# Kernel tuning notes

Hardware: AMD Instinct MI355X
Metric: run time of the kernel (lower is better)

Reference implementation:

```python
import jax, jax.numpy as jnp
import numpy as np

D_MODEL = 64     # input_dim // 4
D_INNER = 128    # expand * d_model
D_STATE = 16
D_CONV = 4
DT_RANK = 4      # ceil(d_model / 16)
EPS = 1e-5


def layernorm(x, g, b):
    m = x.mean(-1, keepdims=True)
    v = x.var(-1, keepdims=True)
    return (x - m) * jax.lax.rsqrt(v + EPS) * g + b


def mamba(u, W_in, W_conv, b_conv, W_xproj, W_dt, b_dt, A_log, Dp, W_out):
    # u: [B, L, d_model]
    B, L, _ = u.shape
    xz = u @ W_in.T                              # [B, L, 2*d_inner]
    xi, z = xz[..., :D_INNER], xz[..., D_INNER:]
    # depthwise causal conv1d over L
    xp = jnp.pad(xi, ((0, 0), (D_CONV - 1, 0), (0, 0)))
    xc = b_conv + sum(xp[:, k:k + L, :] * W_conv[:, k] for k in range(D_CONV))
    xc = jax.nn.silu(xc)                         # [B, L, d_inner]
    proj = xc @ W_xproj.T                        # [B, L, dt_rank + 2*d_state]
    dtp = proj[..., :DT_RANK]
    Bm = proj[..., DT_RANK:DT_RANK + D_STATE]    # [B, L, d_state]
    Cm = proj[..., DT_RANK + D_STATE:]           # [B, L, d_state]
    dt = jax.nn.softplus(dtp @ W_dt.T + b_dt)    # [B, L, d_inner]
    A = -jnp.exp(A_log)                          # [d_inner, d_state]
    dA = jnp.exp(dt[..., None] * A)              # [B, L, d_inner, d_state]
    dBx = (dt * xc)[..., None] * Bm[:, :, None, :]

    def step(h, t):
        dA_t, dBx_t, C_t = t
        h = dA_t * h + dBx_t                     # [B, d_inner, d_state]
        return h, jnp.einsum('bds,bs->bd', h, C_t)

    h0 = jnp.zeros((B, D_INNER, D_STATE), u.dtype)
    _, ys = jax.lax.scan(step, h0, (dA.transpose(1, 0, 2, 3),
                                    dBx.transpose(1, 0, 2, 3),
                                    Cm.transpose(1, 0, 2)))
    y = ys.transpose(1, 0, 2) + Dp * xc          # [B, L, d_inner]
    y = y * jax.nn.silu(z)
    return y @ W_out.T                           # [B, L, d_model]


def _forward(x, x1, x2, x3, g1, be1, g2, be2, g3, be3, g4, be4, skip_scale,
             W_in, W_conv, b_conv, W_xproj, W_dt, b_dt, A_log, D, W_out):
    Bb, C = x.shape[:2]
    img_dims = x2.shape[2:]
    mparams = (W_in, W_conv, b_conv, W_xproj, W_dt, b_dt, A_log, D, W_out)

    def branch(inp, g, b):
        xf = inp.reshape(Bb, C, -1).transpose(0, 2, 1)   # [B, L, C]
        xn = layernorm(xf, g, b)
        return mamba(xn, *mparams) + skip_scale * xn

    x_mamba = jnp.concatenate([branch(x, g1, be1), branch(x1, g2, be2),
                               branch(x2, g3, be3), branch(x3, g4, be4)], axis=2)
    out = x_mamba.transpose(0, 2, 1).reshape(Bb, 4 * C, *img_dims)
    return out


def setup_inputs():
    key = jax.random.key(0)
    ks = jax.random.split(key, 12)
    f = lambda k, shp, s=1.0: jax.random.normal(k, shp, dtype=jnp.float32) * s
    inp = {
        'x': f(ks[0], (8, 64, 32, 32)),
        'x1': f(ks[1], (8, 64, 32, 32)),
        'x2': f(ks[2], (8, 64, 32, 32)),
        'x3': f(ks[3], (8, 64, 32, 32)),
        'g1': jnp.ones(64), 'be1': jnp.zeros(64),
        'g2': jnp.ones(64), 'be2': jnp.zeros(64),
        'g3': jnp.ones(64), 'be3': jnp.zeros(64),
        'g4': jnp.ones(64), 'be4': jnp.zeros(64),
        'skip_scale': jnp.ones((1,), jnp.float32),
        'W_in': f(ks[4], (2 * D_INNER, D_MODEL), 0.1),
        'W_conv': f(ks[5], (D_INNER, D_CONV), 0.3),
        'b_conv': jnp.zeros(D_INNER),
        'W_xproj': f(ks[6], (DT_RANK + 2 * D_STATE, D_INNER), 0.1),
        'W_dt': f(ks[7], (D_INNER, DT_RANK), 0.1),
        'b_dt': f(ks[8], (D_INNER,), 0.1),
        'A_log': jnp.log(jnp.tile(jnp.arange(1, D_STATE + 1, dtype=jnp.float32), (D_INNER, 1))),
        'D': jnp.ones(D_INNER),
        'W_out': f(ks[9], (D_MODEL, D_INNER), 0.1),
    }
    return inp


def reference(x, x1, x2, x3, g1, be1, g2, be2, g3, be3, g4, be4, skip_scale,
              W_in, W_conv, b_conv, W_xproj, W_dt, b_dt, A_log, D, W_out):
    return _forward(x, x1, x2, x3, g1, be1, g2, be2, g3, be3, g4, be4, skip_scale,
                    W_in, W_conv, b_conv, W_xproj, W_dt, b_dt, A_log, D, W_out)
```

## Files before the change

### kernel.cpp

```cpp
#include <hip/hip_runtime.h>
#include <hip/hip_bf16.h>

#define L2E 1.4426950408889634f
#define LN2 0.6931471805599453f

__device__ __forceinline__ float fexp2(float x) { return __builtin_amdgcn_exp2f(x); }
__device__ __forceinline__ float flog2(float x) { return __builtin_amdgcn_logf(x); }
__device__ __forceinline__ int uniform(int x) { return __builtin_amdgcn_readfirstlane(x); }
__device__ __forceinline__ float sigmoidf_(float v) { return 1.f / (1.f + fexp2(-v * L2E)); }
__device__ __forceinline__ float softplusf_(float t) {
    return (t > 20.f) ? t : LN2 * flog2(1.f + fexp2(t * L2E));
}

constexpr size_t O_M   = 0;
constexpr size_t O_RS  = 32768;
constexpr size_t O_G   = 65536;
constexpr size_t O_Z   = 4259840;
constexpr size_t O_XC  = 8454144;
constexpr size_t O_BM  = 12648448;
constexpr size_t O_CM  = 13172736;
constexpr size_t O_DTP = 13697024;
constexpr size_t O_HP  = 13828096;

__global__ __launch_bounds__(256) void k1_ln_inproj(
    const float* __restrict__ x0, const float* __restrict__ x1,
    const float* __restrict__ x2, const float* __restrict__ x3,
    const float* __restrict__ win,
    const float* __restrict__ g1, const float* __restrict__ be1,
    const float* __restrict__ g2, const float* __restrict__ be2,
    const float* __restrict__ g3, const float* __restrict__ be3,
    const float* __restrict__ g4, const float* __restrict__ be4,
    float* __restrict__ ws)
{
    __shared__ float sX[64 * 68];
    __shared__ float sW[64 * 68];
    __shared__ float sM[64], sR[64];
    int bid = blockIdx.x;
    int seq = bid >> 6, jb = (bid >> 4) & 3, pb = bid & 15;
    int branch = seq >> 3, b = seq & 7;
    int tid = threadIdx.x;
    int lane = tid & 63;
    int wq = uniform(tid >> 6);
    const float* xin = (branch==0)?x0:(branch==1)?x1:(branch==2)?x2:x3;
    const float* gam = (branch==0)?g1:(branch==1)?g2:(branch==2)?g3:g4;
    const float* bet = (branch==0)?be1:(branch==1)?be2:(branch==2)?be3:be4;
    const float* xb = xin + (size_t)b * 65536;

#pragma unroll
    for (int r = 0; r < 16; ++r) {
        int row = r * 4 + wq;
        sX[row * 68 + lane] = xb[(size_t)row * 1024 + pb * 64 + lane];
        sW[lane * 68 + row] = win[(size_t)(jb * 64 + row) * 64 + lane];
    }
    __syncthreads();
    if (tid < 64) {
        float sum = 0.f, sq = 0.f;
#pragma unroll
        for (int c = 0; c < 64; ++c) {
            float v = sX[c * 68 + tid];
            sum += v; sq += v * v;
        }
        float mean = sum * (1.f/64.f);
        float var  = sq * (1.f/64.f) - mean * mean;
        float rs   = rsqrtf(var + 1e-5f);
        sM[tid] = mean; sR[tid] = rs;
        if (jb == 0) {
            ws[O_M  + (size_t)seq * 1024 + pb * 64 + tid] = mean;
            ws[O_RS + (size_t)seq * 1024 + pb * 64 + tid] = rs;
        }
    }
    __syncthreads();
#pragma unroll
    for (int r = 0; r < 16; ++r) {
        int c = r * 4 + wq;
        float v = sX[c * 68 + lane];
        sX[c * 68 + lane] = (v - sM[lane]) * sR[lane] * gam[c] + bet[c];
    }
    __syncthreads();
    int jt = tid >> 4, pt = tid & 15;
    float acc[4][4];
#pragma unroll
    for (int i = 0; i < 4; ++i)
#pragma unroll
        for (int j = 0; j < 4; ++j) acc[i][j] = 0.f;
    for (int c = 0; c < 64; ++c) {
        float4 wv = *(const float4*)&sW[c * 68 + jt * 4];
        float4 xv = *(const float4*)&sX[c * 68 + pt * 4];
        float w[4] = {wv.x, wv.y, wv.z, wv.w};
        float x[4] = {xv.x, xv.y, xv.z, xv.w};
#pragma unroll
        for (int i = 0; i < 4; ++i)
#pragma unroll
            for (int j = 0; j < 4; ++j) acc[i][j] += w[i] * x[j];
    }
    int p0 = pb * 64 + pt * 4;
    float* xi = ws + O_G + (size_t)seq * 131072;
    float* zz = ws + O_Z + (size_t)seq * 131072;
#pragma unroll
    for (int ji = 0; ji < 4; ++ji) {
        int j = jb * 64 + jt * 4 + ji;
        float4 v = make_float4(acc[ji][0], acc[ji][1], acc[ji][2], acc[ji][3]);
        if (j < 128) *(float4*)&xi[(size_t)j * 1024 + p0] = v;
        else         *(float4*)&zz[(size_t)(j - 128) * 1024 + p0] = v;
    }
}

__global__ __launch_bounds__(256) void k2_conv_proj(
    const float* __restrict__ wconv, const float* __restrict__ bconv,
    const float* __restrict__ wxp, float* __restrict__ ws)
{
    __shared__ float sWx[128 * 40];
    __shared__ float sAcc[36 * 64];
    int bid = blockIdx.x;
    int seq = bid >> 4, ptile = bid & 15;
    int tid = threadIdx.x;
    int lane = tid & 63;
    int wq = uniform(tid >> 6);
    int p = ptile * 64 + lane;

    for (int i = tid; i < 36 * 64; i += 256) sAcc[i] = 0.f;
    for (int i = tid; i < 36 * 128; i += 256) {
        int j = i >> 7, d = i & 127;
        sWx[d * 40 + j] = wxp[i];
    }
    __syncthreads();

    const float* xirow = ws + O_G  + (size_t)seq * 131072;
    float*       xcrow = ws + O_XC + (size_t)seq * 131072;
    float acc36[36];
#pragma unroll
    for (int j = 0; j < 36; ++j) acc36[j] = 0.f;

    for (int dd = 0; dd < 32; ++dd) {
        int d = wq * 32 + dd;
        const float* row = xirow + (size_t)d * 1024;
        float4 wc = *(const float4*)&wconv[d * 4];
        float v = bconv[d];
        v += ((p >= 3) ? row[p-3] : 0.f) * wc.x;
        v += ((p >= 2) ? row[p-2] : 0.f) * wc.y;
        v += ((p >= 1) ? row[p-1] : 0.f) * wc.z;
        v += row[p] * wc.w;
        v = v * sigmoidf_(v);
        xcrow[(size_t)d * 1024 + p] = v;
#pragma unroll
        for (int jq = 0; jq < 9; ++jq) {
            float4 w4 = *(const float4*)&sWx[d * 40 + jq * 4];
            acc36[jq*4+0] += v * w4.x;
            acc36[jq*4+1] += v * w4.y;
            acc36[jq*4+2] += v * w4.z;
            acc36[jq*4+3] += v * w4.w;
        }
    }
#pragma unroll
    for (int j = 0; j < 36; ++j) atomicAdd(&sAcc[j * 64 + lane], acc36[j]);
    __syncthreads();
    if (tid < 64) {
        int pp = ptile * 64 + tid;
        float* Bm = ws + O_BM + (size_t)seq * 16384;
        float* Cm = ws + O_CM + (size_t)seq * 16384;
        for (int j = 0; j < 36; ++j) {
            float t = sAcc[j * 64 + tid];
            if (j < 4)       ws[O_DTP + ((size_t)seq * 1024 + pp) * 4 + j] = t;
            else if (j < 20) Bm[(size_t)(j - 4)  * 1024 + pp] = t;
            else             Cm[(size_t)(j - 20) * 1024 + pp] = t;
        }
    }
}

__device__ __forceinline__ void k3_preload(const float* wdt, const float* bdt,
                                           const float* alog, int d0, int s0,
                                           float4& wdt0, float4& wdt1, float& bdt0, float& bdt1,
                                           float* a2)
{
    wdt0 = *(const float4*)(wdt + d0 * 4);
    wdt1 = *(const float4*)(wdt + (d0 + 1) * 4);
    bdt0 = bdt[d0]; bdt1 = bdt[d0 + 1];
    float4 a0 = *(const float4*)(alog + d0 * 16 + s0);
    float4 a1 = *(const float4*)(alog + (d0 + 1) * 16 + s0);
    a2[0] = -fexp2(a0.x * L2E) * L2E; a2[1] = -fexp2(a0.y * L2E) * L2E;
    a2[2] = -fexp2(a0.z * L2E) * L2E; a2[3] = -fexp2(a0.w * L2E) * L2E;
    a2[4] = -fexp2(a1.x * L2E) * L2E; a2[5] = -fexp2(a1.y * L2E) * L2E;
    a2[6] = -fexp2(a1.z * L2E) * L2E; a2[7] = -fexp2(a1.w * L2E) * L2E;
}

__global__ __launch_bounds__(256) void k3a_scan(const float* __restrict__ wdt,
                                                const float* __restrict__ bdt,
                                                const float* __restrict__ alog,
                                                float* __restrict__ ws)
{
    __shared__ float sXC[128 * 33];
    __shared__ __align__(16) float sB[32 * 16];
    __shared__ __align__(16) float sDtp[32 * 4];
    int bid = blockIdx.x;
    int seq = bid >> 5, ch = bid & 31;
    int lb = ch * 32;
    int tid = threadIdx.x;
    int d0 = (tid >> 2) * 2, s0 = (tid & 3) * 4;

    float4 wdt0, wdt1; float bdt0, bdt1; float a2[8];
    k3_preload(wdt, bdt, alog, d0, s0, wdt0, wdt1, bdt0, bdt1, a2);

    const float* xcg = ws + O_XC + (size_t)seq * 131072;
    const float* Bmg = ws + O_BM + (size_t)seq * 16384;
    for (int i = tid; i < 4096; i += 256) {
        int d = i >> 5, li = i & 31;
        sXC[d * 33 + li] = xcg[(size_t)d * 1024 + lb + li];
    }
    for (int i = tid; i < 512; i += 256) {
        int s = i >> 5, li = i & 31;
        sB[li * 16 + s] = Bmg[(size_t)s * 1024 + lb + li];
    }
    if (tid < 128) sDtp[tid] = ws[O_DTP + ((size_t)seq * 1024 + lb + (tid >> 2)) * 4 + (tid & 3)];
    __syncthreads();

    float h[8];
#pragma unroll
    for (int i = 0; i < 8; ++i) h[i] = 0.f;
    float sdt0 = 0.f, sdt1 = 0.f;
    for (int li = 0; li < 32; ++li) {
        float4 q = *(const float4*)&sDtp[li * 4];
        float dt0 = softplusf_(bdt0 + q.x*wdt0.x + q.y*wdt0.y + q.z*wdt0.z + q.w*wdt0.w);
        float dt1 = softplusf_(bdt1 + q.x*wdt1.x + q.y*wdt1.y + q.z*wdt1.z + q.w*wdt1.w);
        float xc0 = sXC[d0 * 33 + li], xc1 = sXC[(d0 + 1) * 33 + li];
        float dx0 = dt0 * xc0, dx1 = dt1 * xc1;
        float4 Bv = *(const float4*)&sB[li * 16 + s0];
        float bv[4] = {Bv.x, Bv.y, Bv.z, Bv.w};
        sdt0 += dt0; sdt1 += dt1;
#pragma unroll
        for (int ss = 0; ss < 4; ++ss) {
            float e0 = fexp2(dt0 * a2[ss]);
            h[ss] = e0 * h[ss] + dx0 * bv[ss];
            float e1 = fexp2(dt1 * a2[4 + ss]);
            h[4 + ss] = e1 * h[4 + ss] + dx1 * bv[ss];
        }
    }
    float* hp = ws + O_HP + (size_t)(seq * 32 + ch) * 4096;
#pragma unroll
    for (int ss = 0; ss < 4; ++ss) {
        hp[d0 * 16 + s0 + ss]            = fexp2(a2[ss] * sdt0);
        hp[(d0 + 1) * 16 + s0 + ss]      = fexp2(a2[4 + ss] * sdt1);
        hp[2048 + d0 * 16 + s0 + ss]     = h[ss];
        hp[2048 + (d0 + 1) * 16 + s0 + ss] = h[4 + ss];
    }
}

__global__ __launch_bounds__(256) void k3b_compose(float* __restrict__ ws)
{
    int seq = blockIdx.x;
    int tid = threadIdx.x;
    int d0 = (tid >> 2) * 2, s0 = (tid & 3) * 4;
    int i0 = d0 * 16 + s0, i1 = (d0 + 1) * 16 + s0;
    float h[8];
#pragma unroll
    for (int i = 0; i < 8; ++i) h[i] = 0.f;
    float* hpb = ws + O_HP + (size_t)seq * 32 * 4096;
    for (int c = 0; c < 32; ++c) {
        float* hp = hpb + (size_t)c * 4096;
        float4 P0 = *(const float4*)&hp[i0];
        float4 P1 = *(const float4*)&hp[i1];
        float4 E0 = *(const float4*)&hp[2048 + i0];
        float4 E1 = *(const float4*)&hp[2048 + i1];
        *(float4*)&hp[i0] = make_float4(h[0], h[1], h[2], h[3]);
        *(float4*)&hp[i1] = make_float4(h[4], h[5], h[6], h[7]);
        h[0] = P0.x * h[0] + E0.x; h[1] = P0.y * h[1] + E0.y;
        h[2] = P0.z * h[2] + E0.z; h[3] = P0.w * h[3] + E0.w;
        h[4] = P1.x * h[4] + E1.x; h[5] = P1.y * h[5] + E1.y;
        h[6] = P1.z * h[6] + E1.z; h[7] = P1.w * h[7] + E1.w;
    }
}

__global__ __launch_bounds__(256) void k3c_scan_y(const float* __restrict__ wdt,
                                                  const float* __restrict__ bdt,
                                                  const float* __restrict__ alog,
                                                  float* __restrict__ ws)
{
    __shared__ float sXC[128 * 33];
    __shared__ float sY[128 * 33];
    __shared__ __align__(16) float sB[32 * 16];
    __shared__ __align__(16) float sC[32 * 16];
    __shared__ __align__(16) float sDtp[32 * 4];
    int bid = blockIdx.x;
    int seq = bid >> 5, ch = bid & 31;
    int lb = ch * 32;
    int tid = threadIdx.x;
    int sq = tid & 3;
    int d0 = (tid >> 2) * 2, s0 = sq * 4;

    float4 wdt0, wdt1; float bdt0, bdt1; float a2[8];
    k3_preload(wdt, bdt, alog, d0, s0, wdt0, wdt1, bdt0, bdt1, a2);

    const float* xcg = ws + O_XC + (size_t)seq * 131072;
    const float* Bmg = ws + O_BM + (size_t)seq * 16384;
    const float* Cmg = ws + O_CM + (size_t)seq * 16384;
    float*       gg  = ws + O_G  + (size_t)seq * 131072;
    for (int i = tid; i < 4096; i += 256) {
        int d = i >> 5, li = i & 31;
        sXC[d * 33 + li] = xcg[(size_t)d * 1024 + lb + li];
    }
    for (int i = tid; i < 512; i += 256) {
        int s = i >> 5, li = i & 31;
        sB[li * 16 + s] = Bmg[(size_t)s * 1024 + lb + li];
        sC[li * 16 + s] = Cmg[(size_t)s * 1024 + lb + li];
    }
    if (tid < 128) sDtp[tid] = ws[O_DTP + ((size_t)seq * 1024 + lb + (tid >> 2)) * 4 + (tid & 3)];

    const float* hp = ws + O_HP + (size_t)(seq * 32 + ch) * 4096;
    float4 H0 = *(const float4*)&hp[d0 * 16 + s0];
    float4 H1 = *(const float4*)&hp[(d0 + 1) * 16 + s0];
    float h[8] = {H0.x, H0.y, H0.z, H0.w, H1.x, H1.y, H1.z, H1.w};
    __syncthreads();

    for (int li = 0; li < 32; ++li) {
        float4 q = *(const float4*)&sDtp[li * 4];
        float dt0 = softplusf_(bdt0 + q.x*wdt0.x + q.y*wdt0.y + q.z*wdt0.z + q.w*wdt0.w);
        float dt1 = softplusf_(bdt1 + q.x*wdt1.x + q.y*wdt1.y + q.z*wdt1.z + q.w*wdt1.w);
        float xc0 = sXC[d0 * 33 + li], xc1 = sXC[(d0 + 1) * 33 + li];
        float dx0 = dt0 * xc0, dx1 = dt1 * xc1;
        float4 Bv = *(const float4*)&sB[li * 16 + s0];
        float4 Cv = *(const float4*)&sC[li * 16 + s0];
        float bv[4] = {Bv.x, Bv.y, Bv.z, Bv.w};
        float cv[4] = {Cv.x, Cv.y, Cv.z, Cv.w};
        float acc0 = 0.f, acc1 = 0.f;
#pragma unroll
        for (int ss = 0; ss < 4; ++ss) {
            float e0 = fexp2(dt0 * a2[ss]);
            h[ss] = e0 * h[ss] + dx0 * bv[ss];
            acc0 += h[ss] * cv[ss];
            float e1 = fexp2(dt1 * a2[4 + ss]);
            h[4 + ss] = e1 * h[4 + ss] + dx1 * bv[ss];
            acc1 += h[4 + ss] * cv[ss];
        }
        acc0 += __shfl_xor(acc0, 1); acc0 += __shfl_xor(acc0, 2);
        acc1 += __shfl_xor(acc1, 1); acc1 += __shfl_xor(acc1, 2);
        if (sq == 0) {
            sY[d0 * 33 + li]       = acc0;
            sY[(d0 + 1) * 33 + li] = acc1;
        }
    }
    __syncthreads();
    for (int i = tid; i < 4096; i += 256) {
        int d = i >> 5, li = i & 31;
        gg[(size_t)d * 1024 + lb + li] = sY[d * 33 + li];
    }
}

__global__ __launch_bounds__(256) void k4_out(
    const float* __restrict__ x0, const float* __restrict__ x1,
    const float* __restrict__ x2, const float* __restrict__ x3,
    const float* __restrict__ g1, const float* __restrict__ be1,
    const float* __restrict__ g2, const float* __restrict__ be2,
    const float* __restrict__ g3, const float* __restrict__ be3,
    const float* __restrict__ g4, const float* __restrict__ be4,
    const float* __restrict__ dpar, const float* __restrict__ woutp,
    const float* __restrict__ skipp, const float* __restrict__ ws,
    float* __restrict__ out)
{
    __shared__ float sG[64 * 68];
    __shared__ float sW[64 * 68];
    int bid = blockIdx.x;
    int seq = bid >> 4, pb = bid & 15;
    int branch = seq >> 3, b = seq & 7;
    int tid = threadIdx.x;
    int lane = tid & 63;
    int wq = uniform(tid >> 6);
    int ct = tid >> 4, pt = tid & 15;

    const float* ys = ws + O_G  + (size_t)seq * 131072;
    const float* zz = ws + O_Z  + (size_t)seq * 131072;
    const float* xc = ws + O_XC + (size_t)seq * 131072;

    float acc[4][4];
#pragma unroll
    for (int i = 0; i < 4; ++i)
#pragma unroll
        for (int j = 0; j < 4; ++j) acc[i][j] = 0.f;

    for (int hf = 0; hf < 2; ++hf) {
#pragma unroll
        for (int r = 0; r < 16; ++r) {
            int row = r * 4 + wq;
            sW[lane * 68 + row] = woutp[(size_t)row * 128 + hf * 64 + lane];
            int d = hf * 64 + row;
            size_t off = (size_t)d * 1024 + pb * 64 + lane;
            float yv = ys[off], zv = zz[off], xcv = xc[off];
            sG[row * 68 + lane] = (yv + dpar[d] * xcv) * (zv * sigmoidf_(zv));
        }
        __syncthreads();
        for (int dl = 0; dl < 64; ++dl) {
            float4 wv = *(const float4*)&sW[dl * 68 + ct * 4];
            float4 gv = *(const float4*)&sG[dl * 68 + pt * 4];
            float w[4] = {wv.x, wv.y, wv.z, wv.w};
            float g[4] = {gv.x, gv.y, gv.z, gv.w};
#pragma unroll
            for (int i = 0; i < 4; ++i)
#pragma unroll
                for (int j = 0; j < 4; ++j) acc[i][j] += w[i] * g[j];
        }
        __syncthreads();
    }

    const float* xin = (branch==0)?x0:(branch==1)?x1:(branch==2)?x2:x3;
    const float* gam = (branch==0)?g1:(branch==1)?g2:(branch==2)?g3:g4;
    const float* bet = (branch==0)?be1:(branch==1)?be2:(branch==2)?be3:be4;
    const float* xb = xin + (size_t)b * 65536;
    int p0 = pb * 64 + pt * 4;
    float skipv = skipp[0];
    float4 m4 = *(const float4*)&ws[O_M  + (size_t)seq * 1024 + p0];
    float4 r4 = *(const float4*)&ws[O_RS + (size_t)seq * 1024 + p0];
    float mm[4] = {m4.x, m4.y, m4.z, m4.w};
    float rr[4] = {r4.x, r4.y, r4.z, r4.w};
#pragma unroll
    for (int ci = 0; ci < 4; ++ci) {
        int c = ct * 4 + ci;
        float4 xv = *(const float4*)&xb[(size_t)c * 1024 + p0];
        float xvv[4] = {xv.x, xv.y, xv.z, xv.w};
        float gc = gam[c], bc = bet[c];
        float o[4];
#pragma unroll
        for (int pi = 0; pi < 4; ++pi) {
            float xn = (xvv[pi] - mm[pi]) * rr[pi] * gc + bc;
            o[pi] = acc[ci][pi] + skipv * xn;
        }
        *(float4*)&out[((size_t)b * 256 + branch * 64 + c) * 1024 + p0] =
            make_float4(o[0], o[1], o[2], o[3]);
    }
}

extern "C" void kernel_launch(void* const* d_in, const int* in_sizes, int n_in,
                              void* d_out, int out_size, void* d_ws, size_t ws_size,
                              hipStream_t stream) {
    float* ws = (float*)d_ws;
    auto f = [&](int i) { return (const float*)d_in[i]; };
    hipLaunchKernelGGL(k1_ln_inproj, dim3(2048), dim3(256), 0, stream,
        f(0), f(1), f(2), f(3), f(13),
        f(4), f(5), f(6), f(7), f(8), f(9), f(10), f(11), ws);
    hipLaunchKernelGGL(k2_conv_proj, dim3(512), dim3(256), 0, stream,
        f(14), f(15), f(16), ws);
    hipLaunchKernelGGL(k3a_scan, dim3(1024), dim3(256), 0, stream, f(17), f(18), f(19), ws);
    hipLaunchKernelGGL(k3b_compose, dim3(32), dim3(256), 0, stream, ws);
    hipLaunchKernelGGL(k3c_scan_y, dim3(1024), dim3(256), 0, stream, f(17), f(18), f(19), ws);
    hipLaunchKernelGGL(k4_out, dim3(512), dim3(256), 0, stream,
        f(0), f(1), f(2), f(3),
        f(4), f(5), f(6), f(7), f(8), f(9), f(10), f(11),
        f(20), f(21), f(12), ws, (float*)d_out);
}
```

Measured before the change: 245.1 us.

## Stage conv inputs in LDS and split x_proj outputs across waves

The conv+x_proj kernel now loads each input row tile (with a three-element halo) into shared memory once, computes the causal conv from LDS, and writes the SiLU result back into the same LDS buffer. The x_proj matvec is then restructured so each wave owns 9 of the 36 output channels over all 128 channels, reading weights as uniform scalar loads. This replaces the earlier per-wave partial sums and 36 LDS atomics per thread plus the serialized 64-thread store loop. It adds an extra barrier and a 128x68 LDS buffer, and relies on the weight loads being scalarized.

```diff
diff --git a/kernel.cpp b/kernel.cpp
--- a/kernel.cpp
+++ b/kernel.cpp
@@ -109,61 +109,66 @@
     const float* __restrict__ wconv, const float* __restrict__ bconv,
     const float* __restrict__ wxp, float* __restrict__ ws)
 {
-    __shared__ float sWx[128 * 40];
-    __shared__ float sAcc[36 * 64];
+    __shared__ float sX[128 * 68];
     int bid = blockIdx.x;
     int seq = bid >> 4, ptile = bid & 15;
     int tid = threadIdx.x;
     int lane = tid & 63;
     int wq = uniform(tid >> 6);
-    int p = ptile * 64 + lane;
-
-    for (int i = tid; i < 36 * 64; i += 256) sAcc[i] = 0.f;
-    for (int i = tid; i < 36 * 128; i += 256) {
-        int j = i >> 7, d = i & 127;
-        sWx[d * 40 + j] = wxp[i];
-    }
-    __syncthreads();
+    int p0 = ptile * 64;
+    int p  = p0 + lane;
 
     const float* xirow = ws + O_G  + (size_t)seq * 131072;
     float*       xcrow = ws + O_XC + (size_t)seq * 131072;
-    float acc36[36];
-#pragma unroll
-    for (int j = 0; j < 36; ++j) acc36[j] = 0.f;
-
+
+#pragma unroll 4
+    for (int r = 0; r < 32; ++r) {
+        int d = r * 4 + wq;
+        const float* row = xirow + (size_t)d * 1024;
+        int gp = p0 - 3 + lane;
+        sX[d * 68 + lane] = (gp >= 0) ? row[gp] : 0.f;
+        if (lane < 3) sX[d * 68 + 64 + lane] = row[p0 + 61 + lane];
+    }
+    __syncthreads();
+
+#pragma unroll 2
     for (int dd = 0; dd < 32; ++dd) {
         int d = wq * 32 + dd;
-        const float* row = xirow + (size_t)d * 1024;
         float4 wc = *(const float4*)&wconv[d * 4];
         float v = bconv[d];
-        v += ((p >= 3) ? row[p-3] : 0.f) * wc.x;
-        v += ((p >= 2) ? row[p-2] : 0.f) * wc.y;
-        v += ((p >= 1) ? row[p-1] : 0.f) * wc.z;
-        v += row[p] * wc.w;
+        float* rowl = &sX[d * 68];
+        v += rowl[lane + 0] * wc.x;
+        v += rowl[lane + 1] * wc.y;
+        v += rowl[lane + 2] * wc.z;
+        v += rowl[lane + 3] * wc.w;
         v = v * sigmoidf_(v);
         xcrow[(size_t)d * 1024 + p] = v;
-#pragma unroll
-        for (int jq = 0; jq < 9; ++jq) {
-            float4 w4 = *(const float4*)&sWx[d * 40 + jq * 4];
-            acc36[jq*4+0] += v * w4.x;
-            acc36[jq*4+1] += v * w4.y;
-            acc36[jq*4+2] += v * w4.z;
-            acc36[jq*4+3] += v * w4.w;
-        }
-    }
-#pragma unroll
-    for (int j = 0; j < 36; ++j) atomicAdd(&sAcc[j * 64 + lane], acc36[j]);
-    __syncthreads();
-    if (tid < 64) {
-        int pp = ptile * 64 + tid;
-        float* Bm = ws + O_BM + (size_t)seq * 16384;
-        float* Cm = ws + O_CM + (size_t)seq * 16384;
-        for (int j = 0; j < 36; ++j) {
-            float t = sAcc[j * 64 + tid];
-            if (j < 4)       ws[O_DTP + ((size_t)seq * 1024 + pp) * 4 + j] = t;
-            else if (j < 20) Bm[(size_t)(j - 4)  * 1024 + pp] = t;
-            else             Cm[(size_t)(j - 20) * 1024 + pp] = t;
-        }
+        rowl[lane + 3] = v;
+    }
+    __syncthreads();
+
+    int j0 = uniform(wq * 9);
+    const float* __restrict__ w0 = wxp + (size_t)j0 * 128;
+    float acc[9];
+#pragma unroll
+    for (int jj = 0; jj < 9; ++jj) acc[jj] = 0.f;
+#pragma unroll 4
+    for (int d = 0; d < 128; ++d) {
+        float xcv = sX[d * 68 + 3 + lane];
+#pragma unroll
+        for (int jj = 0; jj < 9; ++jj)
+            acc[jj] += w0[jj * 128 + d] * xcv;
+    }
+
+    float* Bm = ws + O_BM + (size_t)seq * 16384;
+    float* Cm = ws + O_CM + (size_t)seq * 16384;
+#pragma unroll
+    for (int jj = 0; jj < 9; ++jj) {
+        int j = j0 + jj;
+        float t = acc[jj];
+        if (j < 4)       ws[O_DTP + ((size_t)seq * 1024 + p) * 4 + j] = t;
+        else if (j < 20) Bm[(size_t)(j - 4)  * 1024 + p] = t;
+        else             Cm[(size_t)(j - 20) * 1024 + p] = t;
     }
 }
 
```

After: 232.6 us. -5.1%, faster.
